# Performance work log

Measured on AMD Instinct MI355X. Metric: run time of the kernel, lower is better.

Reference implementation:

```python
import jax, jax.numpy as jnp
import numpy as np

_EPS = 1e-12  # torch F.normalize eps


def _normalize(x):
    # x: [B, N, 3]; matches torch.nn.functional.normalize(x, dim=2)
    norm = jnp.linalg.norm(x, axis=2, keepdims=True)
    return x / jnp.maximum(norm, _EPS)


def setup_inputs() -> dict:
    key = jax.random.key(0)
    k1, k2 = jax.random.split(key)
    xyz1 = jax.random.normal(k1, (8, 4096, 6), dtype=jnp.float32)
    xyz2 = jax.random.normal(k2, (8, 4096, 6), dtype=jnp.float32)
    return {"xyz1": xyz1, "xyz2": xyz2}


def reference(xyz1, xyz2):
    p1 = xyz1[:, :, :3]  # [B, N, 3]
    p2 = xyz2[:, :, :3]  # [B, M, 3]
    n1 = xyz1[:, :, 3:]  # [B, N, 3]
    n2 = xyz2[:, :, 3:]  # [B, M, 3]

    # Pairwise squared L2: |a|^2 + |b|^2 - 2 a.b  -> [B, N, M]
    sq1 = jnp.sum(p1 * p1, axis=2)  # [B, N]
    sq2 = jnp.sum(p2 * p2, axis=2)  # [B, M]
    cross = jnp.einsum('bnd,bmd->bnm', p1, p2)
    d = sq1[:, :, None] + sq2[:, None, :] - 2.0 * cross  # [B, N, M]

    dist1 = jnp.min(d, axis=2)      # [B, N] NN of each p1 in p2
    idx1 = jnp.argmin(d, axis=2)    # [B, N]
    dist2 = jnp.min(d, axis=1)      # [B, M] NN of each p2 in p1
    idx2 = jnp.argmin(d, axis=1)    # [B, M]

    # Gather matched normals
    t1 = jnp.take_along_axis(n2, idx1[:, :, None], axis=1)  # [B, N, 3]
    t2 = jnp.take_along_axis(n1, idx2[:, :, None], axis=1)  # [B, M, 3]

    nd1 = jnp.sum((_normalize(n1) - _normalize(t1)) ** 2, axis=2)  # [B, N]
    nd2 = jnp.sum((_normalize(n2) - _normalize(t2)) ** 2, axis=2)  # [B, M]

    return jnp.mean(dist1) + jnp.mean(dist2) + jnp.mean(nd1) + jnp.mean(nd2)
```

## Files before the change

kernel.cpp:

```cpp
#include <hip/hip_runtime.h>
#include <cstdint>

#define NB 8
#define NP 4096

typedef __attribute__((ext_vector_type(8))) short bf16x8;
typedef __attribute__((ext_vector_type(4))) float f32x4;
typedef __attribute__((ext_vector_type(4))) unsigned int u32x4;


__device__ inline void split3(float x, unsigned short& a, unsigned short& b,
                              unsigned short& c) {
    unsigned int xb = __float_as_uint(x);
    float s0 = __uint_as_float(xb & 0xFFFF0000u);
    float r1 = x - s0;
    unsigned int r1b = __float_as_uint(r1);
    float s1 = __uint_as_float(r1b & 0xFFFF0000u);
    float r2 = r1 - s1;
    unsigned int r2b = __float_as_uint(r2);
    a = (unsigned short)(xb >> 16);
    b = (unsigned short)(r1b >> 16);
    c = (unsigned short)(r2b >> 16);
}

__global__ __launch_bounds__(256) void chamfer_prep(
    const float* __restrict__ xyz1, const float* __restrict__ xyz2,
    unsigned int* __restrict__ atab, float* __restrict__ out)
{
    int gid = blockIdx.x * 256 + threadIdx.x;
    if (gid == 0) out[0] = 0.0f;
    int pt  = gid & (NP - 1);
    int b   = (gid >> 12) & 7;
    int set = gid >> 15;

    const float* src = (set ? xyz2 : xyz1) + ((size_t)b * NP + pt) * 6;
    float x = src[0], y = src[1], z = src[2];

    unsigned short sx[3], sy[3], sz[3], sb[3];
    split3(x, sx[0], sx[1], sx[2]);
    split3(y, sy[0], sy[1], sy[2]);
    split3(z, sz[0], sz[1], sz[2]);
    float bias = 0.5f * (x * x + y * y + z * z);
    split3(bias, sb[0], sb[1], sb[2]);

    unsigned short S[32];
    #pragma unroll
    for (int d = 0; d < 3; ++d) {
        #pragma unroll
        for (int i = 0; i < 3; ++i) {
            unsigned short v = (d == 0 ? sx[i] : (d == 1 ? sy[i] : sz[i]));
            v ^= 0x8000;
            #pragma unroll
            for (int j = 0; j < 3; ++j) S[d * 9 + i * 3 + j] = v;
        }
    }
    S[27] = sb[0]; S[28] = sb[1]; S[29] = sb[2];
    S[30] = 0x3F80; S[31] = 0x3F80;

    u32x4* dst = reinterpret_cast<u32x4*>(atab + (size_t)gid * 16);
    #pragma unroll
    for (int m = 0; m < 4; ++m) {
        u32x4 w;
        #pragma unroll
        for (int e = 0; e < 4; ++e) {
            int k = m * 8 + e * 2;
            w[e] = (unsigned int)S[k] | ((unsigned int)S[k + 1] << 16);
        }
        dst[m] = w;
    }
}

__device__ inline void gload_lds16(const unsigned int* g, unsigned int* l) {
    __builtin_amdgcn_global_load_lds(
        (const __attribute__((address_space(1))) unsigned int*)g,
        (__attribute__((address_space(3))) unsigned int*)l, 16, 0, 0);
}

__global__ __launch_bounds__(256) void chamfer_mfma(
    const float* __restrict__ xyz1, const float* __restrict__ xyz2,
    const unsigned int* __restrict__ atab, float* __restrict__ out)
{
    __shared__ unsigned int stage[8192];
    __shared__ unsigned int qbuf[4][16][16];
    __shared__ float wredf[4];

    int bx  = blockIdx.x;
    int qc  = bx & 63;
    int b   = (bx >> 6) & 7;
    int dir = bx >> 9;

    const float* qset = dir ? xyz2 : xyz1;
    const float* tset = dir ? xyz1 : xyz2;
    int tid = threadIdx.x;
    int w   = tid >> 6;
    int l   = tid & 63;
    int col = l & 15;
    int g   = l >> 4;
    int qbase = qc * 64 + w * 16;

    if (l < 16) {
        const float* qs = qset + ((size_t)b * NP + qbase + l) * 6;
        float qx = qs[0], qy = qs[1], qz = qs[2];
        unsigned short sx[3], sy[3], sz[3];
        split3(qx, sx[0], sx[1], sx[2]);
        split3(qy, sy[0], sy[1], sy[2]);
        split3(qz, sz[0], sz[1], sz[2]);
        float qq2 = 0.5f * (qx * qx + qy * qy + qz * qz);
        unsigned int qqb = __float_as_uint(qq2);
        float qh = __uint_as_float(qqb & 0xFFFF0000u);
        unsigned int qlb = __float_as_uint(qq2 - qh);

        unsigned short S[32];
        #pragma unroll
        for (int d = 0; d < 3; ++d)
            #pragma unroll
            for (int i = 0; i < 3; ++i)
                #pragma unroll
                for (int j = 0; j < 3; ++j)
                    S[d * 9 + i * 3 + j] =
                        (d == 0 ? sx[j] : (d == 1 ? sy[j] : sz[j]));
        S[27] = 0x3F80; S[28] = 0x3F80; S[29] = 0x3F80;
        S[30] = (unsigned short)(qqb >> 16);
        S[31] = (unsigned short)(qlb >> 16);
        #pragma unroll
        for (int m = 0; m < 16; ++m)
            qbuf[w][l][m] = (unsigned int)S[2 * m] | ((unsigned int)S[2 * m + 1] << 16);
    }
    __syncthreads();
    bf16x8 bfrag = *reinterpret_cast<const bf16x8*>(&qbuf[w][col][g * 4]);

    const unsigned int* atab_base =
        atab + ((size_t)((1 - dir) * NB + b) * NP) * 16;

    unsigned int p  = 0xFFFFFFFFu;
    unsigned int vX = (unsigned int)(g * 4);
    f32x4 czero = {0.0f, 0.0f, 0.0f, 0.0f};

    for (int s0 = 0; s0 < NP; s0 += 512) {
        const unsigned int* src = atab_base + (size_t)s0 * 16;
        #pragma unroll
        for (int r = 0; r < 8; ++r)
            gload_lds16(src + r * 1024 + tid * 4, &stage[r * 1024 + tid * 4]);
        __syncthreads();

        #pragma unroll 4
        for (int t = 0; t < 32; ++t) {
            bf16x8 af = *reinterpret_cast<const bf16x8*>(
                &stage[(t * 16 + col) * 16 + g * 4]);
            f32x4 D = __builtin_amdgcn_mfma_f32_16x16x32_bf16(af, bfrag, czero, 0, 0, 0);
            unsigned int p0 = (__float_as_uint(D[0]) & 0xFFFFF000u);
            unsigned int p1 = (__float_as_uint(D[1]) & 0xFFFFF000u) | 1u;
            unsigned int p2 = (__float_as_uint(D[2]) & 0xFFFFF000u) | 2u;
            unsigned int p3 = (__float_as_uint(D[3]) & 0xFFFFF000u) | 3u;
            unsigned int pm = min(min(p0, p1), min(p2, p3));
            p = min(p, pm | vX);
            vX += 16u;
        }
        __syncthreads();
    }

    p = min(p, (unsigned int)__shfl_xor((int)p, 16, 64));
    p = min(p, (unsigned int)__shfl_xor((int)p, 32, 64));

    float contrib = 0.0f;
    if (l < 16) {
        int q = qbase + l;
        int idx = (int)(p & 0xFFFu);
        float dist = fmaxf(2.0f * __uint_as_float(p & 0xFFFFF000u), 0.0f);

        const float* nq = qset + ((size_t)b * NP + q) * 6 + 3;
        const float* nt = tset + ((size_t)b * NP + idx) * 6 + 3;
        float ax = nq[0], ay = nq[1], az = nq[2];
        float bxn = nt[0], byn = nt[1], bzn = nt[2];
        float na = fmaxf(sqrtf(ax * ax + ay * ay + az * az), 1e-12f);
        float nb = fmaxf(sqrtf(bxn * bxn + byn * byn + bzn * bzn), 1e-12f);
        float ra = 1.0f / na, rb = 1.0f / nb;
        float dx = ax * ra - bxn * rb;
        float dy = ay * ra - byn * rb;
        float dz = az * ra - bzn * rb;
        float nd = dx * dx + dy * dy + dz * dz;
        contrib = (dist + nd) * (1.0f / 32768.0f);
    }
    #pragma unroll
    for (int off = 1; off < 64; off <<= 1)
        contrib += __shfl_xor(contrib, off, 64);
    if (l == 0) wredf[w] = contrib;
    __syncthreads();
    if (tid == 0)
        atomicAdd(out, wredf[0] + wredf[1] + wredf[2] + wredf[3]);
}

extern "C" void kernel_launch(void* const* d_in, const int* in_sizes, int n_in,
                              void* d_out, int out_size, void* d_ws, size_t ws_size,
                              hipStream_t stream) {
    const float* xyz1 = (const float*)d_in[0];
    const float* xyz2 = (const float*)d_in[1];
    float* out = (float*)d_out;
    unsigned int* atab = (unsigned int*)d_ws;

    chamfer_prep<<<256, 256, 0, stream>>>(xyz1, xyz2, atab, out);
    chamfer_mfma<<<1024, 256, 0, stream>>>(xyz1, xyz2, atab, out);
}
```

Before: 94.83 us.

## Split target range across blocks, double query tiles per wave, add finish kernel

Each block now handles 128 queries against half of the target set. Each wave runs two MFMAs per staged A fragment, so every LDS-staged target tile is reused twice. Per-half argmin packs are written to a workspace buffer, and a new finish kernel merges the two halves, gathers normals and reduces. This halves per-block global-to-LDS traffic per query and shortens the serial loop, at the cost of an extra kernel launch and a partial-result round trip through global memory. Because the 12-bit index field is now relative to a 2048-point half, the half offset is reapplied in the finish kernel.

```diff
diff --git a/kernel.cpp b/kernel.cpp
--- a/kernel.cpp
+++ b/kernel.cpp
@@ -78,28 +78,25 @@
 
 __global__ __launch_bounds__(256) void chamfer_mfma(
     const float* __restrict__ xyz1, const float* __restrict__ xyz2,
-    const unsigned int* __restrict__ atab, float* __restrict__ out)
+    const unsigned int* __restrict__ atab, unsigned int* __restrict__ part)
 {
     __shared__ unsigned int stage[8192];
-    __shared__ unsigned int qbuf[4][16][16];
-    __shared__ float wredf[4];
-
-    int bx  = blockIdx.x;
-    int qc  = bx & 63;
-    int b   = (bx >> 6) & 7;
-    int dir = bx >> 9;
+
+    int bx    = blockIdx.x;
+    int thalf = bx & 1;
+    int qc    = (bx >> 1) & 31;
+    int b     = (bx >> 6) & 7;
+    int dir   = bx >> 9;
 
     const float* qset = dir ? xyz2 : xyz1;
-    const float* tset = dir ? xyz1 : xyz2;
     int tid = threadIdx.x;
     int w   = tid >> 6;
     int l   = tid & 63;
     int col = l & 15;
     int g   = l >> 4;
-    int qbase = qc * 64 + w * 16;
-
-    if (l < 16) {
-        const float* qs = qset + ((size_t)b * NP + qbase + l) * 6;
+
+    if (tid < 128) {
+        const float* qs = qset + ((size_t)b * NP + qc * 128 + tid) * 6;
         float qx = qs[0], qy = qs[1], qz = qs[2];
         unsigned short sx[3], sy[3], sz[3];
         split3(qx, sx[0], sx[1], sx[2]);
@@ -124,20 +121,23 @@
         S[31] = (unsigned short)(qlb >> 16);
         #pragma unroll
         for (int m = 0; m < 16; ++m)
-            qbuf[w][l][m] = (unsigned int)S[2 * m] | ((unsigned int)S[2 * m + 1] << 16);
+            stage[tid * 16 + m] =
+                (unsigned int)S[2 * m] | ((unsigned int)S[2 * m + 1] << 16);
     }
     __syncthreads();
-    bf16x8 bfrag = *reinterpret_cast<const bf16x8*>(&qbuf[w][col][g * 4]);
-
-    const unsigned int* atab_base =
-        atab + ((size_t)((1 - dir) * NB + b) * NP) * 16;
-
-    unsigned int p  = 0xFFFFFFFFu;
+    bf16x8 bf0 = *reinterpret_cast<const bf16x8*>(&stage[(w * 32 + col) * 16 + g * 4]);
+    bf16x8 bf1 = *reinterpret_cast<const bf16x8*>(&stage[(w * 32 + 16 + col) * 16 + g * 4]);
+    __syncthreads();
+
+    const unsigned int* abase =
+        atab + ((size_t)((1 - dir) * NB + b) * NP + thalf * 2048) * 16;
+
+    unsigned int p0r = 0xFFFFFFFFu, p1r = 0xFFFFFFFFu;
     unsigned int vX = (unsigned int)(g * 4);
     f32x4 czero = {0.0f, 0.0f, 0.0f, 0.0f};
 
-    for (int s0 = 0; s0 < NP; s0 += 512) {
-        const unsigned int* src = atab_base + (size_t)s0 * 16;
+    for (int s0 = 0; s0 < 2048; s0 += 512) {
+        const unsigned int* src = abase + (size_t)s0 * 16;
         #pragma unroll
         for (int r = 0; r < 8; ++r)
             gload_lds16(src + r * 1024 + tid * 4, &stage[r * 1024 + tid * 4]);
@@ -147,47 +147,80 @@
         for (int t = 0; t < 32; ++t) {
             bf16x8 af = *reinterpret_cast<const bf16x8*>(
                 &stage[(t * 16 + col) * 16 + g * 4]);
-            f32x4 D = __builtin_amdgcn_mfma_f32_16x16x32_bf16(af, bfrag, czero, 0, 0, 0);
-            unsigned int p0 = (__float_as_uint(D[0]) & 0xFFFFF000u);
-            unsigned int p1 = (__float_as_uint(D[1]) & 0xFFFFF000u) | 1u;
-            unsigned int p2 = (__float_as_uint(D[2]) & 0xFFFFF000u) | 2u;
-            unsigned int p3 = (__float_as_uint(D[3]) & 0xFFFFF000u) | 3u;
-            unsigned int pm = min(min(p0, p1), min(p2, p3));
-            p = min(p, pm | vX);
+            f32x4 D0 = __builtin_amdgcn_mfma_f32_16x16x32_bf16(af, bf0, czero, 0, 0, 0);
+            f32x4 D1 = __builtin_amdgcn_mfma_f32_16x16x32_bf16(af, bf1, czero, 0, 0, 0);
+            unsigned int a0 = (__float_as_uint(D0[0]) & 0xFFFFF000u);
+            unsigned int a1 = (__float_as_uint(D0[1]) & 0xFFFFF000u) | 1u;
+            unsigned int a2 = (__float_as_uint(D0[2]) & 0xFFFFF000u) | 2u;
+            unsigned int a3 = (__float_as_uint(D0[3]) & 0xFFFFF000u) | 3u;
+            unsigned int pm0 = min(min(a0, a1), min(a2, a3));
+            p0r = min(p0r, pm0 | vX);
+            unsigned int c0 = (__float_as_uint(D1[0]) & 0xFFFFF000u);
+            unsigned int c1 = (__float_as_uint(D1[1]) & 0xFFFFF000u) | 1u;
+            unsigned int c2 = (__float_as_uint(D1[2]) & 0xFFFFF000u) | 2u;
+            unsigned int c3 = (__float_as_uint(D1[3]) & 0xFFFFF000u) | 3u;
+            unsigned int pm1 = min(min(c0, c1), min(c2, c3));
+            p1r = min(p1r, pm1 | vX);
             vX += 16u;
         }
         __syncthreads();
     }
 
-    p = min(p, (unsigned int)__shfl_xor((int)p, 16, 64));
-    p = min(p, (unsigned int)__shfl_xor((int)p, 32, 64));
-
-    float contrib = 0.0f;
-    if (l < 16) {
-        int q = qbase + l;
-        int idx = (int)(p & 0xFFFu);
-        float dist = fmaxf(2.0f * __uint_as_float(p & 0xFFFFF000u), 0.0f);
-
-        const float* nq = qset + ((size_t)b * NP + q) * 6 + 3;
-        const float* nt = tset + ((size_t)b * NP + idx) * 6 + 3;
-        float ax = nq[0], ay = nq[1], az = nq[2];
-        float bxn = nt[0], byn = nt[1], bzn = nt[2];
-        float na = fmaxf(sqrtf(ax * ax + ay * ay + az * az), 1e-12f);
-        float nb = fmaxf(sqrtf(bxn * bxn + byn * byn + bzn * bzn), 1e-12f);
-        float ra = 1.0f / na, rb = 1.0f / nb;
-        float dx = ax * ra - bxn * rb;
-        float dy = ay * ra - byn * rb;
-        float dz = az * ra - bzn * rb;
-        float nd = dx * dx + dy * dy + dz * dz;
-        contrib = (dist + nd) * (1.0f / 32768.0f);
-    }
-    #pragma unroll
-    for (int off = 1; off < 64; off <<= 1)
-        contrib += __shfl_xor(contrib, off, 64);
-    if (l == 0) wredf[w] = contrib;
+    p0r = min(p0r, (unsigned int)__shfl_xor((int)p0r, 16, 64));
+    p0r = min(p0r, (unsigned int)__shfl_xor((int)p0r, 32, 64));
+    p1r = min(p1r, (unsigned int)__shfl_xor((int)p1r, 16, 64));
+    p1r = min(p1r, (unsigned int)__shfl_xor((int)p1r, 32, 64));
+
+    if (l < 32) {
+        unsigned int val = (l < 16) ? p0r : p1r;
+        part[(size_t)thalf * (2 * NB * NP) +
+             ((size_t)(dir * NB + b) * NP) + qc * 128 + w * 32 + l] = val;
+    }
+}
+
+__global__ __launch_bounds__(256) void chamfer_finish(
+    const float* __restrict__ xyz1, const float* __restrict__ xyz2,
+    const unsigned int* __restrict__ part, float* __restrict__ out)
+{
+    int gid = blockIdx.x * 256 + threadIdx.x;
+    int q   = gid & (NP - 1);
+    int db  = gid >> 12;
+    int b   = db & 7;
+    int dir = db >> 3;
+
+    unsigned int p0 = part[gid];
+    unsigned int p1 = part[2 * NB * NP + gid];
+    int seg = (p1 < p0) ? 1 : 0;
+    unsigned int p = seg ? p1 : p0;
+
+    const float* qset = dir ? xyz2 : xyz1;
+    const float* tset = dir ? xyz1 : xyz2;
+
+    float dist = fmaxf(2.0f * __uint_as_float(p & 0xFFFFF000u), 0.0f);
+    int j = seg * 2048 + (int)(p & 0xFFFu);
+
+    const float* nq = qset + ((size_t)b * NP + q) * 6 + 3;
+    const float* nt = tset + ((size_t)b * NP + j) * 6 + 3;
+    float ax = nq[0], ay = nq[1], az = nq[2];
+    float bx = nt[0], by = nt[1], bz = nt[2];
+
+    float na = fmaxf(sqrtf(ax * ax + ay * ay + az * az), 1e-12f);
+    float nb = fmaxf(sqrtf(bx * bx + by * by + bz * bz), 1e-12f);
+    float ra = 1.0f / na, rb = 1.0f / nb;
+    float dx = ax * ra - bx * rb;
+    float dy = ay * ra - by * rb;
+    float dz = az * ra - bz * rb;
+    float nd = dx * dx + dy * dy + dz * dz;
+
+    float contrib = (dist + nd) * (1.0f / 32768.0f);
+
+    for (int off = 32; off > 0; off >>= 1)
+        contrib += __shfl_down(contrib, off, 64);
+    __shared__ float wsum[4];
+    if ((threadIdx.x & 63) == 0) wsum[threadIdx.x >> 6] = contrib;
     __syncthreads();
-    if (tid == 0)
-        atomicAdd(out, wredf[0] + wredf[1] + wredf[2] + wredf[3]);
+    if (threadIdx.x == 0)
+        atomicAdd(out, wsum[0] + wsum[1] + wsum[2] + wsum[3]);
 }
 
 extern "C" void kernel_launch(void* const* d_in, const int* in_sizes, int n_in,
@@ -196,8 +229,11 @@
     const float* xyz1 = (const float*)d_in[0];
     const float* xyz2 = (const float*)d_in[1];
     float* out = (float*)d_out;
-    unsigned int* atab = (unsigned int*)d_ws;
+
+    unsigned int* part = (unsigned int*)d_ws;
+    unsigned int* atab = part + 2 * (2 * NB * NP);
 
     chamfer_prep<<<256, 256, 0, stream>>>(xyz1, xyz2, atab, out);
-    chamfer_mfma<<<1024, 256, 0, stream>>>(xyz1, xyz2, atab, out);
-}
+    chamfer_mfma<<<1024, 256, 0, stream>>>(xyz1, xyz2, atab, part);
+    chamfer_finish<<<(2 * NB * NP) / 256, 256, 0, stream>>>(xyz1, xyz2, part, out);
+}
```

Result: faster. 92.89 us (-2.1%).
